# Kernel tuning notes

Measured on AMD Instinct MI355X. Metric: run time of the kernel, lower is better.

The kernel has to match this reference:

```python
import jax, jax.numpy as jnp
import numpy as np

N = 2_097_152          # n_transitions = n_envs * buffer_size
GAMMA = 0.99
GAE_LAMBDA = 0.95
CLIP_EPS = 0.2
NORM_ADVANTAGES = True


def setup_inputs() -> dict:
    key = jax.random.key(0)
    ks = jax.random.split(key, 7)
    f = lambda k: jax.random.normal(k, (N, 1), dtype=jnp.float32)
    return {
        "rewards": f(ks[0]),
        "values": f(ks[1]),
        "next_values": f(ks[2]),
        "log_probs": -jnp.abs(f(ks[3])),       # log-probs are <= 0
        "old_log_probs": -jnp.abs(f(ks[4])),
        "terminated": jax.random.randint(ks[5], (N, 1), 0, 2).astype(bool),
        "truncated": jax.random.randint(ks[6], (N, 1), 0, 2).astype(bool),
    }


def reference(rewards, values, next_values, log_probs, old_log_probs,
              terminated, truncated):
    dtype = rewards.dtype
    dones = jnp.logical_or(terminated, truncated)
    not_term = 1.0 - terminated.astype(dtype)          # [N,1]
    not_done = 1.0 - dones.astype(dtype)               # [N,1]

    # TD residuals: delta_n = r_n + gamma * (1 - terminated_n) * V(s'_n) - V(s_n)
    deltas = rewards + GAMMA * not_term * next_values - values   # [N,1]

    # Reverse GAE recurrence (the torch Python for-loop, fused into one scan):
    # adv_n = (1 - done_n) * gamma * lambda * adv_{n+1} + delta_n
    coef = not_done[:, 0] * (GAMMA * GAE_LAMBDA)       # [N]

    def step(adv, cd):
        c, d = cd
        adv = c * adv + d
        return adv, adv

    _, advantages = jax.lax.scan(step, jnp.zeros((), dtype),
                                 (coef, deltas[:, 0]), reverse=True)
    advantages = advantages[:, None]                   # [N,1]

    lambda_returns = advantages + values               # [N,1]

    if NORM_ADVANTAGES:
        # torch .std() is the unbiased (ddof=1) estimator
        adv_n = (advantages - advantages.mean()) / (
            jnp.std(advantages, ddof=1) + 1e-9)
    else:
        adv_n = advantages

    # PPO clipped surrogate, per-sample (the .mean() is a trivial reduction)
    ratio = jnp.exp(log_probs - old_log_probs)
    clamped = jnp.clip(ratio, 1.0 - CLIP_EPS, 1.0 + CLIP_EPS)
    per_sample_actor_loss = -jnp.minimum(ratio * adv_n, clamped * adv_n)

    # [N,3]: normalized advantages, lambda returns, per-sample clipped objective
    return jnp.concatenate([adv_n, lambda_returns, per_sample_actor_loss], axis=1)
```

## Files before the change

kernel.cpp:

```cpp
#include <hip/hip_runtime.h>
#include <stdint.h>

static constexpr int BLOCK = 256;
static constexpr int ITEMS = 8;
static constexpr int CHUNK = BLOCK * ITEMS;
static constexpr int MAXNB = 1024;

#define GAMMA_F 0.99f
static __device__ __forceinline__ float gl_const() { return (float)(0.99 * 0.95); }

__device__ __forceinline__ int detect_mode(const void* term, int n_elems, int* flg) {
    int t = threadIdx.x;
    if (t == 0) { flg[0] = 0; flg[1] = 0; }
    __syncthreads();
    if (t < 256) {
        const unsigned char* p = (const unsigned char*)term;
        int i0 = 4 * t;
        if (i0 + 3 < n_elems) {
            unsigned b1 = p[i0 + 1], b2 = p[i0 + 2], b3 = p[i0 + 3];
            if (b1) atomicOr(&flg[0], 1);
            if (b2 | b3) atomicOr(&flg[1], 1);
        }
    }
    __syncthreads();
    return flg[0] ? 1 : (flg[1] ? 2 : 0);
}

__device__ __forceinline__ int load_bool1(const void* p, long i, int mode) {
    if (mode == 1) return ((const unsigned char*)p)[i] != 0;
    if (mode == 0) return ((const int*)p)[i] != 0;
    return ((const float*)p)[i] != 0.0f;
}

__device__ __forceinline__ void load_bool8(const void* p, long base, int mode, int* f) {
    if (mode == 1) {
        uint2 q = *(const uint2*)((const unsigned char*)p + base);
        unsigned w[2] = {q.x, q.y};
#pragma unroll
        for (int j = 0; j < 8; ++j) f[j] = (int)((w[j >> 2] >> ((j & 3) * 8)) & 0xffu);
    } else if (mode == 0) {
        const int4* q = (const int4*)((const int*)p + base);
#pragma unroll
        for (int k = 0; k < 2; ++k) {
            int4 v = q[k];
            f[4*k] = v.x; f[4*k+1] = v.y; f[4*k+2] = v.z; f[4*k+3] = v.w;
        }
    } else {
        const float4* q = (const float4*)((const float*)p + base);
#pragma unroll
        for (int k = 0; k < 2; ++k) {
            float4 v = q[k];
            f[4*k] = v.x != 0.f; f[4*k+1] = v.y != 0.f; f[4*k+2] = v.z != 0.f; f[4*k+3] = v.w != 0.f;
        }
    }
}

__device__ __forceinline__ void compute_cd(
    const float* __restrict__ rewards, const float* __restrict__ values,
    const float* __restrict__ next_values, const void* __restrict__ term,
    const void* __restrict__ trunc, int mode, long base, int n,
    float* c, float* d, float* v)
{
    const float GL = gl_const();
    if (base + ITEMS <= n) {
        float r[ITEMS], nv[ITEMS];
        const float4* r4 = (const float4*)(rewards + base);
        const float4* v4 = (const float4*)(values + base);
        const float4* n4 = (const float4*)(next_values + base);
#pragma unroll
        for (int k = 0; k < 2; ++k) {
            float4 a = r4[k]; r[4*k]=a.x; r[4*k+1]=a.y; r[4*k+2]=a.z; r[4*k+3]=a.w;
            float4 b = v4[k]; v[4*k]=b.x; v[4*k+1]=b.y; v[4*k+2]=b.z; v[4*k+3]=b.w;
            float4 q = n4[k]; nv[4*k]=q.x; nv[4*k+1]=q.y; nv[4*k+2]=q.z; nv[4*k+3]=q.w;
        }
        int tm[ITEMS], tr[ITEMS];
        load_bool8(term,  base, mode, tm);
        load_bool8(trunc, base, mode, tr);
#pragma unroll
        for (int j = 0; j < ITEMS; ++j) {
            float nt = tm[j] ? 0.f : 1.f;
            float nd = (tm[j] | tr[j]) ? 0.f : 1.f;
            d[j] = r[j] + GAMMA_F * nt * nv[j] - v[j];
            c[j] = nd * GL;
        }
    } else {
#pragma unroll
        for (int j = 0; j < ITEMS; ++j) {
            long i = base + j;
            if (i < (long)n) {
                int tm = load_bool1(term, i, mode);
                int tr = load_bool1(trunc, i, mode);
                float nt = tm ? 0.f : 1.f;
                float nd = (tm | tr) ? 0.f : 1.f;
                v[j] = values[i];
                d[j] = rewards[i] + GAMMA_F * nt * next_values[i] - v[j];
                c[j] = nd * GL;
            } else { c[j] = 1.f; d[j] = 0.f; v[j] = 0.f; }
        }
    }
}

__global__ __launch_bounds__(BLOCK) void k1_agg(
    const float* __restrict__ rewards, const float* __restrict__ values,
    const float* __restrict__ next_values, const void* __restrict__ term,
    const void* __restrict__ trunc, float2* __restrict__ blockAgg,
    float4* __restrict__ bs4, float* __restrict__ bs1, int n)
{
    __shared__ int flg[2];
    __shared__ float sA[BLOCK], sB[BLOCK], sC[BLOCK], sD[BLOCK], sE[BLOCK];
    int mode = detect_mode(term, n, flg);
    int t = threadIdx.x;
    long base = (long)blockIdx.x * CHUNK + (long)t * ITEMS;
    float c[ITEMS], d[ITEMS], v[ITEMS];
    compute_cd(rewards, values, next_values, term, trunc, mode, base, n, c, d, v);
    float a = 1.f, b = 0.f;
#pragma unroll
    for (int j = ITEMS - 1; j >= 0; --j) { b = c[j]*b + d[j]; a = c[j]*a; }
    sA[t] = a; sB[t] = b;
    __syncthreads();
    for (int dd = 1; dd < BLOCK; dd <<= 1) {
        float ra = 1.f, rb = 0.f;
        if (t + dd < BLOCK) { ra = sA[t + dd]; rb = sB[t + dd]; }
        __syncthreads();
        b = a * rb + b;
        a = a * ra;
        sA[t] = a; sB[t] = b;
        __syncthreads();
    }
    float p = 1.f, q = 0.f;
    if (t + 1 < BLOCK) { p = sA[t + 1]; q = sB[t + 1]; }
    if (t == 0) blockAgg[blockIdx.x] = make_float2(a, b);
    float sP = 0.f, sQ = 0.f, sP2 = 0.f, sPQ = 0.f, sQ2 = 0.f;
#pragma unroll
    for (int j = ITEMS - 1; j >= 0; --j) {
        p = c[j] * p;
        q = c[j] * q + d[j];
        if (base + j < (long)n) {
            sP += p; sQ += q; sP2 += p*p; sPQ += p*q; sQ2 += q*q;
        }
    }
    __syncthreads();
    sA[t] = sP; sB[t] = sQ; sC[t] = sP2; sD[t] = sPQ; sE[t] = sQ2;
    __syncthreads();
    for (int dd = BLOCK / 2; dd > 0; dd >>= 1) {
        if (t < dd) {
            sA[t] += sA[t + dd]; sB[t] += sB[t + dd]; sC[t] += sC[t + dd];
            sD[t] += sD[t + dd]; sE[t] += sE[t + dd];
        }
        __syncthreads();
    }
    if (t == 0) {
        bs4[blockIdx.x] = make_float4(sA[0], sB[0], sC[0], sD[0]);
        bs1[blockIdx.x] = sE[0];
    }
}

__global__ __launch_bounds__(BLOCK) void k2_scan(
    const float2* __restrict__ blockAgg, const float4* __restrict__ bs4,
    const float* __restrict__ bs1, float* __restrict__ S,
    float* __restrict__ stats, int nb, int n)
{
    __shared__ float sA[BLOCK], sB[BLOCK];
    __shared__ double dS[BLOCK], dS2[BLOCK];
    const int t = threadIdx.x;
    float la[4], lb[4];
#pragma unroll
    for (int j = 0; j < 4; ++j) {
        int i = 4 * t + j;
        if (i < nb) { float2 f = blockAgg[i]; la[j] = f.x; lb[j] = f.y; }
        else        { la[j] = 1.f; lb[j] = 0.f; }
    }
    float a = 1.f, b = 0.f;
#pragma unroll
    for (int j = 3; j >= 0; --j) { b = la[j] * b + lb[j]; a = la[j] * a; }
    sA[t] = a; sB[t] = b;
    __syncthreads();
    for (int dd = 1; dd < BLOCK; dd <<= 1) {
        float ra = 1.f, rb = 0.f;
        if (t + dd < BLOCK) { ra = sA[t + dd]; rb = sB[t + dd]; }
        __syncthreads();
        b = a * rb + b;
        a = a * ra;
        sA[t] = a; sB[t] = b;
        __syncthreads();
    }
    float x = (t + 1 < BLOCK) ? sB[t + 1] : 0.f;
    double ds = 0.0, ds2 = 0.0;
#pragma unroll
    for (int j = 3; j >= 0; --j) {
        int i = 4 * t + j;
        if (i < nb) {
            S[i] = x;
            float4 s4 = bs4[i];
            double xd = (double)x;
            ds  += (double)s4.x * xd + (double)s4.y;
            ds2 += (double)s4.z * xd * xd + 2.0 * (double)s4.w * xd + (double)bs1[i];
        }
        x = la[j] * x + lb[j];
    }
    dS[t] = ds; dS2[t] = ds2;
    __syncthreads();
    for (int dd = BLOCK / 2; dd > 0; dd >>= 1) {
        if (t < dd) { dS[t] += dS[t + dd]; dS2[t] += dS2[t + dd]; }
        __syncthreads();
    }
    if (t == 0) {
        double sum = dS[0], sumsq = dS2[0];
        double mean = sum / (double)n;
        double var = (sumsq - sum * sum / (double)n) / (double)(n - 1);
        if (var < 0.0) var = 0.0;
        stats[0] = (float)mean;
        stats[1] = 1.0f / ((float)sqrt(var) + 1e-9f);
    }
}

__global__ __launch_bounds__(BLOCK) void k3_final(
    const float* __restrict__ rewards, const float* __restrict__ values,
    const float* __restrict__ next_values, const void* __restrict__ term,
    const void* __restrict__ trunc, const float* __restrict__ lp,
    const float* __restrict__ olp, const float* __restrict__ S,
    const float* __restrict__ stats, float* __restrict__ out, int n)
{
    __shared__ int flg[2];
    __shared__ float sA[BLOCK], sB[BLOCK];
    int mode = detect_mode(term, n, flg);
    int t = threadIdx.x;
    long base = (long)blockIdx.x * CHUNK + (long)t * ITEMS;
    float c[ITEMS], d[ITEMS], v[ITEMS];
    compute_cd(rewards, values, next_values, term, trunc, mode, base, n, c, d, v);
    float a = 1.f, b = 0.f;
#pragma unroll
    for (int j = ITEMS - 1; j >= 0; --j) { b = c[j]*b + d[j]; a = c[j]*a; }
    sA[t] = a; sB[t] = b;
    __syncthreads();
    for (int dd = 1; dd < BLOCK; dd <<= 1) {
        float ra = 1.f, rb = 0.f;
        if (t + dd < BLOCK) { ra = sA[t + dd]; rb = sB[t + dd]; }
        __syncthreads();
        b = a * rb + b;
        a = a * ra;
        sA[t] = a; sB[t] = b;
        __syncthreads();
    }
    float ea = 1.f, eb = 0.f;
    if (t + 1 < BLOCK) { ea = sA[t + 1]; eb = sB[t + 1]; }
    float x = ea * S[blockIdx.x] + eb;
    float adv[ITEMS];
#pragma unroll
    for (int j = ITEMS - 1; j >= 0; --j) {
        x = c[j] * x + d[j];
        adv[j] = x;
    }
    const float mean = stats[0];
    const float inv  = stats[1];
    if (base + ITEMS <= n) {
        float l[ITEMS], o[ITEMS];
        const float4* l4 = (const float4*)(lp + base);
        const float4* o4 = (const float4*)(olp + base);
#pragma unroll
        for (int k = 0; k < 2; ++k) {
            float4 q = l4[k]; l[4*k]=q.x; l[4*k+1]=q.y; l[4*k+2]=q.z; l[4*k+3]=q.w;
            float4 w = o4[k]; o[4*k]=w.x; o[4*k+1]=w.y; o[4*k+2]=w.z; o[4*k+3]=w.w;
        }
        float buf[3 * ITEMS];
#pragma unroll
        for (int j = 0; j < ITEMS; ++j) {
            float an = (adv[j] - mean) * inv;
            float ratio = expf(l[j] - o[j]);
            float cl = fminf(fmaxf(ratio, 0.8f), 1.2f);
            buf[3*j]     = an;
            buf[3*j + 1] = adv[j] + v[j];
            buf[3*j + 2] = -fminf(ratio * an, cl * an);
        }
        float4* dst = (float4*)(out + 3 * base);
#pragma unroll
        for (int k = 0; k < 6; ++k)
            dst[k] = make_float4(buf[4*k], buf[4*k+1], buf[4*k+2], buf[4*k+3]);
    } else {
        for (int j = 0; j < ITEMS; ++j) {
            long i = base + j;
            if (i < (long)n) {
                float an = (adv[j] - mean) * inv;
                float ratio = expf(lp[i] - olp[i]);
                float cl = fminf(fmaxf(ratio, 0.8f), 1.2f);
                out[3*i]     = an;
                out[3*i + 1] = adv[j] + v[j];
                out[3*i + 2] = -fminf(ratio * an, cl * an);
            }
        }
    }
}

extern "C" void kernel_launch(void* const* d_in, const int* in_sizes, int n_in,
                              void* d_out, int out_size, void* d_ws, size_t ws_size,
                              hipStream_t stream) {
    const float* rewards     = (const float*)d_in[0];
    const float* values      = (const float*)d_in[1];
    const float* next_values = (const float*)d_in[2];
    const float* lp          = (const float*)d_in[3];
    const float* olp         = (const float*)d_in[4];
    const void*  term        = d_in[5];
    const void*  trunc       = d_in[6];
    float* out = (float*)d_out;
    int n = in_sizes[0];
    int nb = (n + CHUNK - 1) / CHUNK;

    char* ws = (char*)d_ws;
    float2* blockAgg = (float2*)ws;
    float4* bs4      = (float4*)(ws + MAXNB * 8);
    float*  bs1      = (float*) (ws + MAXNB * 8 + MAXNB * 16);
    float*  S        = (float*) (ws + MAXNB * 8 + MAXNB * 16 + MAXNB * 4);
    float*  stats    = (float*) (ws + MAXNB * 8 + MAXNB * 16 + MAXNB * 4 + MAXNB * 4);

    k1_agg <<<nb, BLOCK, 0, stream>>>(rewards, values, next_values, term, trunc,
                                      blockAgg, bs4, bs1, n);
    k2_scan<<<1,  BLOCK, 0, stream>>>(blockAgg, bs4, bs1, S, stats, nb, n);
    k3_final<<<nb, BLOCK, 0, stream>>>(rewards, values, next_values, term, trunc,
                                       lp, olp, S, stats, out, n);
}
```

Measured before the change: 130.9 us.

## Fold block-scan pass into last-block tail and cache per-thread carries

The separate single-block scan and statistics kernel is removed. Its work now runs in the last block to finish the first kernel, chosen with an atomic ticket counter and thread fences. The intra-block scan and reductions now use wave-level shuffles instead of LDS loops with many barriers. Each thread's exclusive carry is written to workspace, so the final kernel no longer repeats the block scan. Output stores become nontemporal. The costs are an extra 4 MB carry buffer written and read back, and a counter reset that relies on the workspace holding a known poison pattern. If the harness does not re-poison the workspace between calls, repeated calls could fail.

```diff
diff --git a/kernel.cpp b/kernel.cpp
--- a/kernel.cpp
+++ b/kernel.cpp
@@ -5,9 +5,17 @@
 static constexpr int ITEMS = 8;
 static constexpr int CHUNK = BLOCK * ITEMS;
 static constexpr int MAXNB = 1024;
+static constexpr unsigned POISON32 = 0xAAAAAAAAu;
+
+typedef float f4v __attribute__((ext_vector_type(4)));
 
 #define GAMMA_F 0.99f
 static __device__ __forceinline__ float gl_const() { return (float)(0.99 * 0.95); }
+
+__device__ __forceinline__ void compose(float& a1, float& b1, float a2, float b2) {
+    b1 = fmaf(a1, b2, b1);
+    a1 = a1 * a2;
+}
 
 __device__ __forceinline__ int detect_mode(const void* term, int n_elems, int* flg) {
     int t = threadIdx.x;
@@ -104,84 +112,105 @@
     const float* __restrict__ rewards, const float* __restrict__ values,
     const float* __restrict__ next_values, const void* __restrict__ term,
     const void* __restrict__ trunc, float2* __restrict__ blockAgg,
-    float4* __restrict__ bs4, float* __restrict__ bs1, int n)
+    float2* __restrict__ E2, float4* __restrict__ bs4, float* __restrict__ bs1,
+    float* __restrict__ S, float* __restrict__ stats,
+    unsigned* __restrict__ counter, int n, int nb)
 {
     __shared__ int flg[2];
-    __shared__ float sA[BLOCK], sB[BLOCK], sC[BLOCK], sD[BLOCK], sE[BLOCK];
-    int mode = detect_mode(term, n, flg);
-    int t = threadIdx.x;
-    long base = (long)blockIdx.x * CHUNK + (long)t * ITEMS;
+    __shared__ float wA[4], wB[4];
+    __shared__ float red[4][5];
+    __shared__ int isLast;
+    __shared__ float sA[BLOCK], sB[BLOCK];
+    __shared__ double dS[BLOCK], dS2[BLOCK];
+
+    const int t = threadIdx.x;
+    const int lane = t & 63, w = t >> 6;
+    const int bid = blockIdx.x;
+    const int mode = detect_mode(term, n, flg);
+    const long base = (long)bid * CHUNK + (long)t * ITEMS;
+
     float c[ITEMS], d[ITEMS], v[ITEMS];
     compute_cd(rewards, values, next_values, term, trunc, mode, base, n, c, d, v);
+
     float a = 1.f, b = 0.f;
 #pragma unroll
-    for (int j = ITEMS - 1; j >= 0; --j) { b = c[j]*b + d[j]; a = c[j]*a; }
-    sA[t] = a; sB[t] = b;
+    for (int j = ITEMS - 1; j >= 0; --j) { b = fmaf(c[j], b, d[j]); a *= c[j]; }
+
+#pragma unroll
+    for (int dd = 1; dd < 64; dd <<= 1) {
+        float ra = __shfl_down(a, dd, 64);
+        float rb = __shfl_down(b, dd, 64);
+        if (lane + dd < 64) { b = fmaf(a, rb, b); a *= ra; }
+    }
+    if (lane == 0) { wA[w] = a; wB[w] = b; }
+    float ea = __shfl_down(a, 1, 64);
+    float eb = __shfl_down(b, 1, 64);
+    if (lane == 63) { ea = 1.f; eb = 0.f; }
+    __syncthreads();
+    for (int ww = w + 1; ww < 4; ++ww) compose(ea, eb, wA[ww], wB[ww]);
+    if (t == 0) {
+        float Aa = wA[0], Ab = wB[0];
+        for (int ww = 1; ww < 4; ++ww) compose(Aa, Ab, wA[ww], wB[ww]);
+        blockAgg[bid] = make_float2(Aa, Ab);
+    }
+    E2[(long)bid * BLOCK + t] = make_float2(ea, eb);
+
+    float p = ea, q = eb;
+    float sP = 0.f, sQ = 0.f, sP2 = 0.f, sPQ = 0.f, sQ2 = 0.f;
+#pragma unroll
+    for (int j = ITEMS - 1; j >= 0; --j) {
+        p = c[j] * p;
+        q = fmaf(c[j], q, d[j]);
+        if (base + j < (long)n) {
+            sP += p; sQ += q; sP2 += p*p; sPQ += p*q; sQ2 += q*q;
+        }
+    }
+#pragma unroll
+    for (int dd = 32; dd > 0; dd >>= 1) {
+        sP  += __shfl_down(sP,  dd, 64);
+        sQ  += __shfl_down(sQ,  dd, 64);
+        sP2 += __shfl_down(sP2, dd, 64);
+        sPQ += __shfl_down(sPQ, dd, 64);
+        sQ2 += __shfl_down(sQ2, dd, 64);
+    }
+    if (lane == 0) { red[w][0]=sP; red[w][1]=sQ; red[w][2]=sP2; red[w][3]=sPQ; red[w][4]=sQ2; }
+    __syncthreads();
+    if (t == 0) {
+        float m0=0,m1=0,m2=0,m3=0,m4=0;
+        for (int ww = 0; ww < 4; ++ww) { m0+=red[ww][0]; m1+=red[ww][1]; m2+=red[ww][2]; m3+=red[ww][3]; m4+=red[ww][4]; }
+        bs4[bid] = make_float4(m0, m1, m2, m3);
+        bs1[bid] = m4;
+    }
+
+    __threadfence();
+    if (t == 0) {
+        atomicCAS(counter, POISON32, 0u);
+        unsigned ticket = atomicAdd(counter, 1u);
+        isLast = (ticket == (unsigned)(nb - 1));
+    }
+    __syncthreads();
+    if (!isLast) return;
+    __threadfence();
+
+    float la[4], lb[4];
+#pragma unroll
+    for (int j = 0; j < 4; ++j) {
+        int i = 4 * t + j;
+        if (i < nb) { float2 f = blockAgg[i]; la[j] = f.x; lb[j] = f.y; }
+        else        { la[j] = 1.f; lb[j] = 0.f; }
+    }
+    float ga = 1.f, gb = 0.f;
+#pragma unroll
+    for (int j = 3; j >= 0; --j) { gb = fmaf(la[j], gb, lb[j]); ga *= la[j]; }
+    sA[t] = ga; sB[t] = gb;
     __syncthreads();
     for (int dd = 1; dd < BLOCK; dd <<= 1) {
         float ra = 1.f, rb = 0.f;
         if (t + dd < BLOCK) { ra = sA[t + dd]; rb = sB[t + dd]; }
         __syncthreads();
-        b = a * rb + b;
-        a = a * ra;
-        sA[t] = a; sB[t] = b;
-        __syncthreads();
-    }
-    float p = 1.f, q = 0.f;
-    if (t + 1 < BLOCK) { p = sA[t + 1]; q = sB[t + 1]; }
-    if (t == 0) blockAgg[blockIdx.x] = make_float2(a, b);
-    float sP = 0.f, sQ = 0.f, sP2 = 0.f, sPQ = 0.f, sQ2 = 0.f;
-#pragma unroll
-    for (int j = ITEMS - 1; j >= 0; --j) {
-        p = c[j] * p;
-        q = c[j] * q + d[j];
-        if (base + j < (long)n) {
-            sP += p; sQ += q; sP2 += p*p; sPQ += p*q; sQ2 += q*q;
-        }
-    }
-    __syncthreads();
-    sA[t] = sP; sB[t] = sQ; sC[t] = sP2; sD[t] = sPQ; sE[t] = sQ2;
-    __syncthreads();
-    for (int dd = BLOCK / 2; dd > 0; dd >>= 1) {
-        if (t < dd) {
-            sA[t] += sA[t + dd]; sB[t] += sB[t + dd]; sC[t] += sC[t + dd];
-            sD[t] += sD[t + dd]; sE[t] += sE[t + dd];
-        }
-        __syncthreads();
-    }
-    if (t == 0) {
-        bs4[blockIdx.x] = make_float4(sA[0], sB[0], sC[0], sD[0]);
-        bs1[blockIdx.x] = sE[0];
-    }
-}
-
-__global__ __launch_bounds__(BLOCK) void k2_scan(
-    const float2* __restrict__ blockAgg, const float4* __restrict__ bs4,
-    const float* __restrict__ bs1, float* __restrict__ S,
-    float* __restrict__ stats, int nb, int n)
-{
-    __shared__ float sA[BLOCK], sB[BLOCK];
-    __shared__ double dS[BLOCK], dS2[BLOCK];
-    const int t = threadIdx.x;
-    float la[4], lb[4];
-#pragma unroll
-    for (int j = 0; j < 4; ++j) {
-        int i = 4 * t + j;
-        if (i < nb) { float2 f = blockAgg[i]; la[j] = f.x; lb[j] = f.y; }
-        else        { la[j] = 1.f; lb[j] = 0.f; }
-    }
-    float a = 1.f, b = 0.f;
-#pragma unroll
-    for (int j = 3; j >= 0; --j) { b = la[j] * b + lb[j]; a = la[j] * a; }
-    sA[t] = a; sB[t] = b;
-    __syncthreads();
-    for (int dd = 1; dd < BLOCK; dd <<= 1) {
-        float ra = 1.f, rb = 0.f;
-        if (t + dd < BLOCK) { ra = sA[t + dd]; rb = sB[t + dd]; }
-        __syncthreads();
-        b = a * rb + b;
-        a = a * ra;
-        sA[t] = a; sB[t] = b;
+        gb = fmaf(ga, rb, gb);
+        ga *= ra;
+        sA[t] = ga; sB[t] = gb;
         __syncthreads();
     }
     float x = (t + 1 < BLOCK) ? sB[t + 1] : 0.f;
@@ -196,7 +225,7 @@
             ds  += (double)s4.x * xd + (double)s4.y;
             ds2 += (double)s4.z * xd * xd + 2.0 * (double)s4.w * xd + (double)bs1[i];
         }
-        x = la[j] * x + lb[j];
+        x = fmaf(la[j], x, lb[j]);
     }
     dS[t] = ds; dS2[t] = ds2;
     __syncthreads();
@@ -218,37 +247,25 @@
     const float* __restrict__ rewards, const float* __restrict__ values,
     const float* __restrict__ next_values, const void* __restrict__ term,
     const void* __restrict__ trunc, const float* __restrict__ lp,
-    const float* __restrict__ olp, const float* __restrict__ S,
-    const float* __restrict__ stats, float* __restrict__ out, int n)
+    const float* __restrict__ olp, const float2* __restrict__ E2,
+    const float* __restrict__ S, const float* __restrict__ stats,
+    float* __restrict__ out, int n)
 {
     __shared__ int flg[2];
-    __shared__ float sA[BLOCK], sB[BLOCK];
-    int mode = detect_mode(term, n, flg);
-    int t = threadIdx.x;
-    long base = (long)blockIdx.x * CHUNK + (long)t * ITEMS;
+    const int t = threadIdx.x;
+    const int bid = blockIdx.x;
+    const int mode = detect_mode(term, n, flg);
+    const long base = (long)bid * CHUNK + (long)t * ITEMS;
+
     float c[ITEMS], d[ITEMS], v[ITEMS];
     compute_cd(rewards, values, next_values, term, trunc, mode, base, n, c, d, v);
-    float a = 1.f, b = 0.f;
-#pragma unroll
-    for (int j = ITEMS - 1; j >= 0; --j) { b = c[j]*b + d[j]; a = c[j]*a; }
-    sA[t] = a; sB[t] = b;
-    __syncthreads();
-    for (int dd = 1; dd < BLOCK; dd <<= 1) {
-        float ra = 1.f, rb = 0.f;
-        if (t + dd < BLOCK) { ra = sA[t + dd]; rb = sB[t + dd]; }
-        __syncthreads();
-        b = a * rb + b;
-        a = a * ra;
-        sA[t] = a; sB[t] = b;
-        __syncthreads();
-    }
-    float ea = 1.f, eb = 0.f;
-    if (t + 1 < BLOCK) { ea = sA[t + 1]; eb = sB[t + 1]; }
-    float x = ea * S[blockIdx.x] + eb;
+
+    float2 e = E2[(long)bid * BLOCK + t];
+    float x = fmaf(e.x, S[bid], e.y);
     float adv[ITEMS];
 #pragma unroll
     for (int j = ITEMS - 1; j >= 0; --j) {
-        x = c[j] * x + d[j];
+        x = fmaf(c[j], x, d[j]);
         adv[j] = x;
     }
     const float mean = stats[0];
@@ -272,10 +289,12 @@
             buf[3*j + 1] = adv[j] + v[j];
             buf[3*j + 2] = -fminf(ratio * an, cl * an);
         }
-        float4* dst = (float4*)(out + 3 * base);
-#pragma unroll
-        for (int k = 0; k < 6; ++k)
-            dst[k] = make_float4(buf[4*k], buf[4*k+1], buf[4*k+2], buf[4*k+3]);
+        f4v* dst = (f4v*)(out + 3 * base);
+#pragma unroll
+        for (int k = 0; k < 6; ++k) {
+            f4v val = { buf[4*k], buf[4*k+1], buf[4*k+2], buf[4*k+3] };
+            __builtin_nontemporal_store(val, dst + k);
+        }
     } else {
         for (int j = 0; j < ITEMS; ++j) {
             long i = base + j;
@@ -306,15 +325,16 @@
     int nb = (n + CHUNK - 1) / CHUNK;
 
     char* ws = (char*)d_ws;
-    float2* blockAgg = (float2*)ws;
-    float4* bs4      = (float4*)(ws + MAXNB * 8);
-    float*  bs1      = (float*) (ws + MAXNB * 8 + MAXNB * 16);
-    float*  S        = (float*) (ws + MAXNB * 8 + MAXNB * 16 + MAXNB * 4);
-    float*  stats    = (float*) (ws + MAXNB * 8 + MAXNB * 16 + MAXNB * 4 + MAXNB * 4);
+    float2*   blockAgg = (float2*)ws;
+    float4*   bs4      = (float4*)(ws + MAXNB * 8);
+    float*    bs1      = (float*) (ws + MAXNB * 8 + MAXNB * 16);
+    float*    S        = (float*) (ws + MAXNB * 8 + MAXNB * 16 + MAXNB * 4);
+    float*    stats    = (float*) (ws + MAXNB * 8 + MAXNB * 16 + MAXNB * 8);
+    unsigned* counter  = (unsigned*)(ws + MAXNB * 8 + MAXNB * 16 + MAXNB * 8 + 64);
+    float2*   E2       = (float2*)(ws + MAXNB * 8 + MAXNB * 16 + MAXNB * 8 + 256);
 
     k1_agg <<<nb, BLOCK, 0, stream>>>(rewards, values, next_values, term, trunc,
-                                      blockAgg, bs4, bs1, n);
-    k2_scan<<<1,  BLOCK, 0, stream>>>(blockAgg, bs4, bs1, S, stats, nb, n);
+                                      blockAgg, E2, bs4, bs1, S, stats, counter, n, nb);
     k3_final<<<nb, BLOCK, 0, stream>>>(rewards, values, next_values, term, trunc,
-                                       lp, olp, S, stats, out, n);
-}
+                                       lp, olp, E2, S, stats, out, n);
+}
```

After: 240.7 us. +83.8%, slower.
